# Optimization experiments

Measured on AMD Instinct MI355X. Metric: run time of the kernel, lower is better.

Reference implementation:

```python
import jax, jax.numpy as jnp
import numpy as np
import math

D_EMBED = 128   # per-head dim (config.d_embed)
N_HEADS = 12
ROPE_BASE = 10000.0


def rope(x):
    # x: [B, H, S, D]; interleaved-pair rotary embedding on last dim
    B, H, S, D = x.shape
    half = D // 2
    inv_freq = 1.0 / (ROPE_BASE ** (jnp.arange(0, half, dtype=jnp.float32) * 2.0 / D))
    ang = jnp.arange(S, dtype=jnp.float32)[:, None] * inv_freq[None, :]  # [S, D/2]
    cos, sin = jnp.cos(ang), jnp.sin(ang)
    xp = x.reshape(B, H, S, half, 2)
    x1, x2 = xp[..., 0], xp[..., 1]
    o1 = x1 * cos - x2 * sin
    o2 = x1 * sin + x2 * cos
    return jnp.stack([o1, o2], axis=-1).reshape(B, H, S, D)


def setup_inputs() -> dict:
    key = jax.random.key(0)
    ks = jax.random.split(key, 5)
    B, S, E = 2, 2048, D_EMBED // 2
    inner = N_HEADS * D_EMBED
    sc = 0.02
    return {
        "q": jax.random.normal(ks[0], (B, S, E), dtype=jnp.float32),
        "Wq": jax.random.normal(ks[1], (inner, E), dtype=jnp.float32) * sc,
        "Wk": jax.random.normal(ks[2], (inner, E), dtype=jnp.float32) * sc,
        "Wv": jax.random.normal(ks[3], (inner, E), dtype=jnp.float32) * sc,
        "Wo": jax.random.normal(ks[4], (E, inner), dtype=jnp.float32) * sc,
    }


def reference(q, Wq, Wk, Wv, Wo):
    B, S, E = q.shape
    H, D = N_HEADS, D_EMBED
    scale = 1.0 / math.sqrt(D)

    def proj(x, W):
        return (x @ W.T).reshape(B, S, H, D).transpose(0, 2, 1, 3)  # [B,H,S,D]

    qh = rope(proj(q, Wq))
    kh = rope(proj(q, Wk))
    vh = proj(q, Wv)

    scores = jnp.einsum("bhsd,bhtd->bhst", qh, kh) * scale  # [B,H,S,S]
    causal = jnp.tril(jnp.ones((S, S), dtype=bool))
    scores = jnp.where(causal, scores, -jnp.inf)
    probs = jax.nn.softmax(scores, axis=-1)  # dropout omitted (eval mode)
    out = jnp.einsum("bhst,bhtd->bhsd", probs, vh)
    out = out.transpose(0, 2, 1, 3).reshape(B, S, H * D)
    return out @ Wo.T  # [B,S,E]
```

## Files before the change

### kernel.cpp

```cpp
#include <hip/hip_runtime.h>
#include <stdint.h>


typedef short v8s __attribute__((ext_vector_type(8)));
typedef unsigned int v4u __attribute__((ext_vector_type(4)));
typedef float v4f __attribute__((ext_vector_type(4)));
typedef float v16f __attribute__((ext_vector_type(16)));

#define MFMA16(a, b, c) __builtin_amdgcn_mfma_f32_16x16x32_bf16(a, b, c, 0, 0, 0)
#define MFMA32(a, b, c) __builtin_amdgcn_mfma_f32_32x32x16_bf16(a, b, c, 0, 0, 0)

#if __has_builtin(__builtin_amdgcn_exp2f)
#define EXP2(x) __builtin_amdgcn_exp2f(x)
#else
#define EXP2(x) exp2f(x)
#endif

#define SCALE2 (0.08838834764831845f * 1.4426950408889634f)

__device__ __forceinline__ unsigned short f2bf(float f) {
  uint32_t u = __builtin_bit_cast(uint32_t, f);
  u += 0x7FFFu + ((u >> 16) & 1u);
  return (unsigned short)(u >> 16);
}

__device__ __forceinline__ uint32_t packbf(float lo, float hi) {
  return __builtin_amdgcn_perm(__builtin_bit_cast(uint32_t, hi) + 0x8000u,
                               __builtin_bit_cast(uint32_t, lo) + 0x8000u,
                               0x07060302u);
}

__device__ __forceinline__ v16f zero16() {
  v16f z;
#pragma unroll
  for (int i = 0; i < 16; ++i) z[i] = 0.f;
  return z;
}

__device__ __forceinline__ void gl_lds16(const unsigned short* g, unsigned short* l) {
  __builtin_amdgcn_global_load_lds(
      (const __attribute__((address_space(1))) uint32_t*)g,
      (__attribute__((address_space(3))) uint32_t*)l, 16, 0, 0);
}

__global__ __launch_bounds__(256) void rope_table(float* __restrict__ cos_t,
                                                  float* __restrict__ sin_t) {
  int idx = blockIdx.x * 256 + threadIdx.x;
  if (idx >= 2048 * 64) return;
  int s = idx >> 6, f = idx & 63;
  float inv = exp2f((float)f * -0.20762050593046014f);
  float ang = (float)s * inv;
  float si, co;
  sincosf(ang, &si, &co);
  cos_t[idx] = co;
  sin_t[idx] = si;
}

__global__ __launch_bounds__(256) void proj_rope(
    const float* __restrict__ x, const float* __restrict__ Wq,
    const float* __restrict__ Wk, const float* __restrict__ Wv,
    const float* __restrict__ cos_t, const float* __restrict__ sin_t,
    unsigned short* __restrict__ qh, unsigned short* __restrict__ kh,
    unsigned short* __restrict__ vt) {
  const int wave = threadIdx.x >> 6, lane = threadIdx.x & 63;
  const int l16 = lane & 15, quad = lane >> 4;
  const int by = blockIdx.y;
  const int o_base = by * 64 + wave * 16;
  const int mat = o_base / 1536;
  const int inner0 = o_base % 1536;
  const int d0w = inner0 & 127;
  const float* Wsrc = (mat == 0) ? Wq : ((mat == 1) ? Wk : Wv);
  const float qscale = (mat == 0) ? SCALE2 : 1.0f;

  __shared__ __align__(16) unsigned short Lt[64][72];

  v8s wb[2];
  {
    const float* wr = Wsrc + (size_t)(inner0 + l16) * 64 + quad * 8;
#pragma unroll
    for (int s = 0; s < 2; ++s) {
      float4 a = *(const float4*)(wr + s * 32);
      float4 b = *(const float4*)(wr + s * 32 + 4);
      v8s t;
      t[0] = (short)f2bf(a.x); t[1] = (short)f2bf(a.y);
      t[2] = (short)f2bf(a.z); t[3] = (short)f2bf(a.w);
      t[4] = (short)f2bf(b.x); t[5] = (short)f2bf(b.y);
      t[6] = (short)f2bf(b.z); t[7] = (short)f2bf(b.w);
      wb[s] = t;
    }
  }

  const int d = d0w + l16;
  const int half = d >> 1;

#pragma unroll
  for (int i = 0; i < 4; ++i) {
    const int tok0 = blockIdx.x * 64 + i * 16;
    const float* xr = x + (size_t)(tok0 + l16) * 64 + quad * 8;
    v8s xa[2];
#pragma unroll
    for (int s = 0; s < 2; ++s) {
      float4 a = *(const float4*)(xr + s * 32);
      float4 b = *(const float4*)(xr + s * 32 + 4);
      v8s t;
      t[0] = (short)f2bf(a.x); t[1] = (short)f2bf(a.y);
      t[2] = (short)f2bf(a.z); t[3] = (short)f2bf(a.w);
      t[4] = (short)f2bf(b.x); t[5] = (short)f2bf(b.y);
      t[6] = (short)f2bf(b.z); t[7] = (short)f2bf(b.w);
      xa[s] = t;
    }
    v4f acc = {0.f, 0.f, 0.f, 0.f};
    acc = MFMA16(xa[0], wb[0], acc);
    acc = MFMA16(xa[1], wb[1], acc);

    if (mat < 2) {
#pragma unroll
      for (int r = 0; r < 4; ++r) {
        int sidx = (tok0 + quad * 4 + r) & 2047;
        float val = acc[r];
        float prt = __shfl_xor(val, 1);
        float co = cos_t[sidx * 64 + half];
        float si = sin_t[sidx * 64 + half];
        float rot = ((d & 1) == 0) ? (val * co - prt * si)
                                   : (prt * si + val * co);
        Lt[i * 16 + quad * 4 + r][wave * 16 + l16] = f2bf(rot * qscale);
      }
    } else {
#pragma unroll
      for (int r = 0; r < 4; ++r)
        Lt[wave * 16 + l16][i * 16 + quad * 4 + r] = f2bf(acc[r]);
    }
  }
  __syncthreads();

  const int matb = (by * 64) / 1536;
  const int innerb = (by * 64) % 1536;
  const int hb = innerb >> 7;
  const int d0b = innerb & 127;
  const int b = (blockIdx.x * 64) >> 11;
  const int tokbase = (blockIdx.x * 64) & 2047;
#pragma unroll
  for (int jj = 0; jj < 2; ++jj) {
    int cid = jj * 256 + threadIdx.x;
    int outer = cid >> 3, ic = cid & 7;
    v8s val = *(const v8s*)&Lt[outer][ic * 8];
    if (matb < 2) {
      unsigned short* dst = (matb == 0 ? qh : kh) +
          (((size_t)(b * 12 + hb)) * 2048 + tokbase + outer) * 128 + d0b + ic * 8;
      *(v8s*)dst = val;
    } else {
      const int kt = tokbase >> 6;
      const int G = ic >> 1, hhb = ic & 1;
      const int dd = d0b + outer;
      unsigned short* dst = vt +
          ((((((size_t)(b * 12 + hb)) * 32 + kt) * 4 + G) * 4 + (dd >> 5)) * 64 +
           hhb * 32 + (dd & 31)) * 8;
      *(v8s*)dst = val;
    }
  }
}

__global__ __launch_bounds__(256, 2) void attn(
    const unsigned short* __restrict__ qh, const unsigned short* __restrict__ kh,
    const unsigned short* __restrict__ vtf, unsigned short* __restrict__ att,
    const float* __restrict__ Wo, unsigned short* __restrict__ wob) {
  const int bh = blockIdx.x;
  const int qb = 15 - (int)blockIdx.y;
  const int t = threadIdx.x;
  const int lane = t & 63;
  const int l31 = lane & 31, hh = lane >> 5;
  const int w = t >> 6;
  const int r0w = qb * 128 + w * 32;
  const int qrow = r0w + l31;
  const int rowmax = r0w + 31;

  const unsigned short* Qb = qh + (size_t)bh * 2048 * 128;
  const unsigned short* Kb = kh + (size_t)bh * 2048 * 128;
  const unsigned short* Vb = vtf + (size_t)bh * 262144;

  __shared__ __align__(16) unsigned short Ktile[3][64 * 128];

  v8s qa[8];
  {
    const unsigned short* qr = Qb + (size_t)(r0w + l31) * 128 + hh * 8;
#pragma unroll
    for (int ks = 0; ks < 8; ++ks) qa[ks] = *(const v8s*)(qr + ks * 16);
  }

  int offK[4], ldsO[4];
#pragma unroll
  for (int i = 0; i < 4; ++i) {
    int flat = i * 256 + t;
    int kr = flat >> 4, kc = flat & 15;
    offK[i] = kr * 128 + ((kc ^ (kr & 15)) << 3);
    ldsO[i] = flat << 3;
  }
  auto stageK = [&](int kt, int buf) {
    const unsigned short* kg = Kb + ((size_t)(kt << 6)) * 128;
#pragma unroll
    for (int i = 0; i < 4; ++i) gl_lds16(kg + offK[i], &Ktile[buf][ldsO[i]]);
  };

  v16f O[4];
#pragma unroll
  for (int i = 0; i < 4; ++i) O[i] = zero16();
  float lsum = 0.f;

  const int nkt = 2 * qb + 2;
  stageK(0, 0);
  stageK(1, 1);
  asm volatile("s_waitcnt vmcnt(4)" ::: "memory");

  for (int kt = 0; kt < nkt; ++kt) {
    __builtin_amdgcn_s_barrier();
    __builtin_amdgcn_sched_barrier(0);
    const int key0 = kt << 6;
    const bool active = key0 <= rowmax;
    const bool hi = (key0 + 32) <= rowmax;

    v8s v0a[4], v0b[4], v1a[4], v1b[4];
    if (active) {
      const unsigned short* Vt = Vb + (size_t)kt * 8192;
#pragma unroll
      for (int dt = 0; dt < 4; ++dt)
        v0a[dt] = *(const v8s*)(Vt + ((0 * 4 + dt) * 64 + lane) * 8);
#pragma unroll
      for (int dt = 0; dt < 4; ++dt)
        v0b[dt] = *(const v8s*)(Vt + ((1 * 4 + dt) * 64 + lane) * 8);
      if (hi) {
#pragma unroll
        for (int dt = 0; dt < 4; ++dt)
          v1a[dt] = *(const v8s*)(Vt + ((2 * 4 + dt) * 64 + lane) * 8);
#pragma unroll
        for (int dt = 0; dt < 4; ++dt)
          v1b[dt] = *(const v8s*)(Vt + ((3 * 4 + dt) * 64 + lane) * 8);
      }
    }
    __builtin_amdgcn_sched_barrier(0);

    if (kt + 2 < nkt) stageK(kt + 2, (kt + 2) % 3);
    __builtin_amdgcn_sched_barrier(0);

    if (!active) {
      if (kt + 2 < nkt) asm volatile("s_waitcnt vmcnt(4)" ::: "memory");
      else              asm volatile("s_waitcnt vmcnt(0)" ::: "memory");
      continue;
    }

    const unsigned short* Kl = Ktile[kt % 3];
    const bool mask0 = (key0 + 31) > r0w;
    const bool mask1 = (key0 + 63) > r0w;

    auto softpack = [&](const v16f& SS, const v16f& ST, int kh2, bool needmask,
                        uint32_t* W) {
#pragma unroll
      for (int m = 0; m < 8; ++m) {
        float pa = EXP2(SS[2 * m] + ST[2 * m]);
        float pb = EXP2(SS[2 * m + 1] + ST[2 * m + 1]);
        if (needmask) {
          int keyb = key0 + kh2 * 32 + 2 * (m & 1) + 8 * (m >> 1) + 4 * hh;
          pa = (keyb <= qrow) ? pa : 0.f;
          pb = (keyb + 1 <= qrow) ? pb : 0.f;
        }
        lsum += pa + pb;
        W[m] = packbf(pa, pb);
      }
    };
    auto pvhalf = [&](const uint32_t* W, int kh2, const v8s* vA, const v8s* vB) {
      uint32_t r0 = __shfl_xor(hh ? W[0] : W[2], 32);
      uint32_t r1 = __shfl_xor(hh ? W[1] : W[3], 32);
      uint32_t r2 = __shfl_xor(hh ? W[4] : W[6], 32);
      uint32_t r3 = __shfl_xor(hh ? W[5] : W[7], 32);
#pragma unroll
      for (int gl = 0; gl < 2; ++gl) {
        const int g = kh2 * 2 + gl;
        if (key0 + g * 16 > rowmax) continue;
        uint32_t rA = gl ? r2 : r0, rB = gl ? r3 : r1;
        v4u fw;
        fw.x = hh ? rA : W[4 * gl];
        fw.y = hh ? rB : W[4 * gl + 1];
        fw.z = hh ? W[4 * gl + 2] : rA;
        fw.w = hh ? W[4 * gl + 3] : rB;
        v8s pfrag = __builtin_bit_cast(v8s, fw);
        const v8s* vv = gl ? vB : vA;
        __builtin_amdgcn_s_setprio(1);
#pragma unroll
        for (int dt = 0; dt < 4; ++dt) O[dt] = MFMA32(vv[dt], pfrag, O[dt]);
        __builtin_amdgcn_s_setprio(0);
      }
    };

    v16f Sa = zero16(), Sb = zero16();
    __builtin_amdgcn_s_setprio(1);
#pragma unroll
    for (int ks = 0; ks < 8; ks += 2) {
      v8s ka0 = *(const v8s*)(
          Kl + ((l31 * 16 + ((2 * ks + hh) ^ (l31 & 15))) << 3));
      v8s ka1 = *(const v8s*)(
          Kl + ((l31 * 16 + ((2 * ks + 2 + hh) ^ (l31 & 15))) << 3));
      Sa = MFMA32(ka0, qa[ks], Sa);
      Sb = MFMA32(ka1, qa[ks + 1], Sb);
    }
    __builtin_amdgcn_s_setprio(0);
    uint32_t W0[8];
    softpack(Sa, Sb, 0, mask0, W0);
    pvhalf(W0, 0, v0a, v0b);

    if (hi) {
      v16f Sc = zero16(), Sd = zero16();
      __builtin_amdgcn_s_setprio(1);
#pragma unroll
      for (int ks = 0; ks < 8; ks += 2) {
        v8s ka0 = *(const v8s*)(
            Kl + (((32 + l31) * 16 + ((2 * ks + hh) ^ (l31 & 15))) << 3));
        v8s ka1 = *(const v8s*)(
            Kl + (((32 + l31) * 16 + ((2 * ks + 2 + hh) ^ (l31 & 15))) << 3));
        Sc = MFMA32(ka0, qa[ks], Sc);
        Sd = MFMA32(ka1, qa[ks + 1], Sd);
      }
      __builtin_amdgcn_s_setprio(0);
      uint32_t W1[8];
      softpack(Sc, Sd, 1, mask1, W1);
      pvhalf(W1, 1, v1a, v1b);
    }
  }

  float tot = lsum + __shfl_xor(lsum, 32);
  float inv = 1.0f / tot;
  const int b = bh / 12, hq = bh % 12;
  unsigned short* arow = att + ((size_t)b * 2048 + qrow) * 1536 + hq * 128;
#pragma unroll
  for (int dt = 0; dt < 4; ++dt) {
#pragma unroll
    for (int pr = 0; pr < 4; ++pr) {
      float a0 = O[dt][4 * pr + 0] * inv, a1 = O[dt][4 * pr + 1] * inv;
      float a2 = O[dt][4 * pr + 2] * inv, a3 = O[dt][4 * pr + 3] * inv;
      uint2 uu;
      uu.x = packbf(a0, a1);
      uu.y = packbf(a2, a3);
      *(uint2*)(arow + dt * 32 + 8 * pr + 4 * hh) = uu;
    }
  }

  if (qb == 0) {
    const int base = bh * 4096;
#pragma unroll
    for (int i = 0; i < 16; ++i) wob[base + i * 256 + t] = f2bf(Wo[base + i * 256 + t]);
  }
}

__global__ __launch_bounds__(256) void outproj(
    const unsigned short* __restrict__ att, const unsigned short* __restrict__ wob,
    float* __restrict__ out) {
  const int wave = threadIdx.x >> 6, lane = threadIdx.x & 63;
  const int l16 = lane & 15, quad = lane >> 4;
  const int tok0 = blockIdx.x * 16;
  const int e0 = wave * 16;

  v4f acc0 = {0.f, 0.f, 0.f, 0.f}, acc1 = {0.f, 0.f, 0.f, 0.f};
  const unsigned short* ar = att + (size_t)(tok0 + l16) * 1536 + quad * 8;
  const unsigned short* wr = wob + (size_t)(e0 + l16) * 1536 + quad * 8;
#pragma unroll 4
  for (int s = 0; s < 24; ++s) {
    v8s a0 = *(const v8s*)(ar + (2 * s) * 32);
    v8s b0 = *(const v8s*)(wr + (2 * s) * 32);
    v8s a1 = *(const v8s*)(ar + (2 * s + 1) * 32);
    v8s b1 = *(const v8s*)(wr + (2 * s + 1) * 32);
    acc0 = MFMA16(a0, b0, acc0);
    acc1 = MFMA16(a1, b1, acc1);
  }
#pragma unroll
  for (int r = 0; r < 4; ++r)
    out[(size_t)(tok0 + quad * 4 + r) * 64 + e0 + l16] = acc0[r] + acc1[r];
}

extern "C" void kernel_launch(void* const* d_in, const int* in_sizes, int n_in,
                              void* d_out, int out_size, void* d_ws,
                              size_t ws_size, hipStream_t stream) {
  const float* q  = (const float*)d_in[0];
  const float* Wq = (const float*)d_in[1];
  const float* Wk = (const float*)d_in[2];
  const float* Wv = (const float*)d_in[3];
  const float* Wo = (const float*)d_in[4];
  float* out = (float*)d_out;

  unsigned short* ws = (unsigned short*)d_ws;
  unsigned short* qh  = ws;
  unsigned short* kh  = ws + 6291456;
  unsigned short* vtf = ws + 12582912;
  unsigned short* att = ws + 18874368;
  float* cos_t = (float*)((char*)d_ws + 50331648);
  float* sin_t = cos_t + 131072;
  unsigned short* wob = (unsigned short*)cos_t;

  rope_table<<<512, 256, 0, stream>>>(cos_t, sin_t);
  proj_rope<<<dim3(64, 72), 256, 0, stream>>>(q, Wq, Wk, Wv, cos_t, sin_t,
                                              qh, kh, vtf);
  attn<<<dim3(24, 16), 256, 0, stream>>>(qh, kh, vtf, att, Wo, wob);
  outproj<<<256, 256, 0, stream>>>(att, wob, out);
}
```

Baseline: 200.9 us.

## Split attention KV range across two wave groups with LDS reduction

Doubles the attention block to 512 threads: two groups of four waves each process half of the causal key tiles for the same 128 query rows, with each group staging its own K tiles into LDS. The partial O accumulators and row sums from the second group are written to swizzled LDS and added by the first group before normalisation and the bf16 store. This halves the serial key-loop length per block to reduce latency on the long causal rows, at the cost of more LDS, a full vmcnt(0) wait every iteration (less prefetch overlap), and an extra reduction step.

After: 424.4 us. 111% more time.

```diff
diff --git a/kernel.cpp b/kernel.cpp
--- a/kernel.cpp
+++ b/kernel.cpp
@@ -160,7 +160,7 @@
   }
 }
 
-__global__ __launch_bounds__(256, 2) void attn(
+__global__ __launch_bounds__(512, 4) void attn(
     const unsigned short* __restrict__ qh, const unsigned short* __restrict__ kh,
     const unsigned short* __restrict__ vtf, unsigned short* __restrict__ att,
     const float* __restrict__ Wo, unsigned short* __restrict__ wob) {
@@ -170,7 +170,8 @@
   const int lane = t & 63;
   const int l31 = lane & 31, hh = lane >> 5;
   const int w = t >> 6;
-  const int r0w = qb * 128 + w * 32;
+  const int rg = w & 3, kherd = w >> 2;
+  const int r0w = qb * 128 + rg * 32;
   const int qrow = r0w + l31;
   const int rowmax = r0w + 31;
 
@@ -178,27 +179,28 @@
   const unsigned short* Kb = kh + (size_t)bh * 2048 * 128;
   const unsigned short* Vb = vtf + (size_t)bh * 262144;
 
-  __shared__ __align__(16) unsigned short Ktile[3][64 * 128];
+  __shared__ __align__(16) unsigned short KSH[4 * 8192 + 512];
 
   v8s qa[8];
   {
-    const unsigned short* qr = Qb + (size_t)(r0w + l31) * 128 + hh * 8;
+    const unsigned short* qr = Qb + (size_t)qrow * 128 + hh * 8;
 #pragma unroll
     for (int ks = 0; ks < 8; ++ks) qa[ks] = *(const v8s*)(qr + ks * 16);
   }
 
-  int offK[4], ldsO[4];
-#pragma unroll
-  for (int i = 0; i < 4; ++i) {
-    int flat = i * 256 + t;
+  int offK[2];
+#pragma unroll
+  for (int i2 = 0; i2 < 2; ++i2) {
+    int flat = i2 * 512 + t;
     int kr = flat >> 4, kc = flat & 15;
-    offK[i] = kr * 128 + ((kc ^ (kr & 15)) << 3);
-    ldsO[i] = flat << 3;
-  }
-  auto stageK = [&](int kt, int buf) {
-    const unsigned short* kg = Kb + ((size_t)(kt << 6)) * 128;
-#pragma unroll
-    for (int i = 0; i < 4; ++i) gl_lds16(kg + offK[i], &Ktile[buf][ldsO[i]]);
+    offK[i2] = kr * 128 + ((kc ^ (kr & 15)) << 3);
+  }
+  auto stageT = [&](int ktile, int slot) {
+    const unsigned short* kg = Kb + ((size_t)(ktile << 6)) * 128;
+    unsigned short* db = &KSH[slot * 8192];
+#pragma unroll
+    for (int i2 = 0; i2 < 2; ++i2)
+      gl_lds16(kg + offK[i2], db + ((i2 * 512 + t) << 3));
   };
 
   v16f O[4];
@@ -206,14 +208,15 @@
   for (int i = 0; i < 4; ++i) O[i] = zero16();
   float lsum = 0.f;
 
-  const int nkt = 2 * qb + 2;
-  stageK(0, 0);
-  stageK(1, 1);
-  asm volatile("s_waitcnt vmcnt(4)" ::: "memory");
-
-  for (int kt = 0; kt < nkt; ++kt) {
+  const int NS = qb + 1;
+  stageT(0, 0);
+  stageT(qb + 1, 2);
+  asm volatile("s_waitcnt vmcnt(0)" ::: "memory");
+
+  for (int i = 0; i < NS; ++i) {
     __builtin_amdgcn_s_barrier();
     __builtin_amdgcn_sched_barrier(0);
+    const int kt = kherd ? (qb + 1 + i) : i;
     const int key0 = kt << 6;
     const bool active = key0 <= rowmax;
     const bool hi = (key0 + 32) <= rowmax;
@@ -238,114 +241,140 @@
     }
     __builtin_amdgcn_sched_barrier(0);
 
-    if (kt + 2 < nkt) stageK(kt + 2, (kt + 2) % 3);
+    if (i + 1 < NS) {
+      stageT(i + 1, (i + 1) & 1);
+      stageT(qb + 2 + i, 2 + ((i + 1) & 1));
+    }
     __builtin_amdgcn_sched_barrier(0);
 
-    if (!active) {
-      if (kt + 2 < nkt) asm volatile("s_waitcnt vmcnt(4)" ::: "memory");
-      else              asm volatile("s_waitcnt vmcnt(0)" ::: "memory");
-      continue;
-    }
-
-    const unsigned short* Kl = Ktile[kt % 3];
-    const bool mask0 = (key0 + 31) > r0w;
-    const bool mask1 = (key0 + 63) > r0w;
-
-    auto softpack = [&](const v16f& SS, const v16f& ST, int kh2, bool needmask,
-                        uint32_t* W) {
-#pragma unroll
-      for (int m = 0; m < 8; ++m) {
-        float pa = EXP2(SS[2 * m] + ST[2 * m]);
-        float pb = EXP2(SS[2 * m + 1] + ST[2 * m + 1]);
-        if (needmask) {
-          int keyb = key0 + kh2 * 32 + 2 * (m & 1) + 8 * (m >> 1) + 4 * hh;
-          pa = (keyb <= qrow) ? pa : 0.f;
-          pb = (keyb + 1 <= qrow) ? pb : 0.f;
+    if (active) {
+      const unsigned short* Kl = &KSH[(kherd * 2 + (i & 1)) * 8192];
+      const bool mask0 = (key0 + 31) > r0w;
+      const bool mask1 = (key0 + 63) > r0w;
+
+      auto softpack = [&](const v16f& SS, const v16f& ST, int kh2, bool needmask,
+                          uint32_t* W) {
+#pragma unroll
+        for (int m = 0; m < 8; ++m) {
+          float pa = EXP2(SS[2 * m] + ST[2 * m]);
+          float pb = EXP2(SS[2 * m + 1] + ST[2 * m + 1]);
+          if (needmask) {
+            int keyb = key0 + kh2 * 32 + 2 * (m & 1) + 8 * (m >> 1) + 4 * hh;
+            pa = (keyb <= qrow) ? pa : 0.f;
+            pb = (keyb + 1 <= qrow) ? pb : 0.f;
+          }
+          lsum += pa + pb;
+          W[m] = packbf(pa, pb);
         }
-        lsum += pa + pb;
-        W[m] = packbf(pa, pb);
-      }
-    };
-    auto pvhalf = [&](const uint32_t* W, int kh2, const v8s* vA, const v8s* vB) {
-      uint32_t r0 = __shfl_xor(hh ? W[0] : W[2], 32);
-      uint32_t r1 = __shfl_xor(hh ? W[1] : W[3], 32);
-      uint32_t r2 = __shfl_xor(hh ? W[4] : W[6], 32);
-      uint32_t r3 = __shfl_xor(hh ? W[5] : W[7], 32);
-#pragma unroll
-      for (int gl = 0; gl < 2; ++gl) {
-        const int g = kh2 * 2 + gl;
-        if (key0 + g * 16 > rowmax) continue;
-        uint32_t rA = gl ? r2 : r0, rB = gl ? r3 : r1;
-        v4u fw;
-        fw.x = hh ? rA : W[4 * gl];
-        fw.y = hh ? rB : W[4 * gl + 1];
-        fw.z = hh ? W[4 * gl + 2] : rA;
-        fw.w = hh ? W[4 * gl + 3] : rB;
-        v8s pfrag = __builtin_bit_cast(v8s, fw);
-        const v8s* vv = gl ? vB : vA;
-        __builtin_amdgcn_s_setprio(1);
-#pragma unroll
-        for (int dt = 0; dt < 4; ++dt) O[dt] = MFMA32(vv[dt], pfrag, O[dt]);
-        __builtin_amdgcn_s_setprio(0);
-      }
-    };
-
-    v16f Sa = zero16(), Sb = zero16();
-    __builtin_amdgcn_s_setprio(1);
-#pragma unroll
-    for (int ks = 0; ks < 8; ks += 2) {
-      v8s ka0 = *(const v8s*)(
-          Kl + ((l31 * 16 + ((2 * ks + hh) ^ (l31 & 15))) << 3));
-      v8s ka1 = *(const v8s*)(
-          Kl + ((l31 * 16 + ((2 * ks + 2 + hh) ^ (l31 & 15))) << 3));
-      Sa = MFMA32(ka0, qa[ks], Sa);
-      Sb = MFMA32(ka1, qa[ks + 1], Sb);
-    }
-    __builtin_amdgcn_s_setprio(0);
-    uint32_t W0[8];
-    softpack(Sa, Sb, 0, mask0, W0);
-    pvhalf(W0, 0, v0a, v0b);
-
-    if (hi) {
-      v16f Sc = zero16(), Sd = zero16();
+      };
+      auto pvhalf = [&](const uint32_t* W, int kh2, const v8s* vA, const v8s* vB) {
+        uint32_t r0 = __shfl_xor(hh ? W[0] : W[2], 32);
+        uint32_t r1 = __shfl_xor(hh ? W[1] : W[3], 32);
+        uint32_t r2 = __shfl_xor(hh ? W[4] : W[6], 32);
+        uint32_t r3 = __shfl_xor(hh ? W[5] : W[7], 32);
+#pragma unroll
+        for (int gl = 0; gl < 2; ++gl) {
+          const int g = kh2 * 2 + gl;
+          if (key0 + g * 16 > rowmax) continue;
+          uint32_t rA = gl ? r2 : r0, rB = gl ? r3 : r1;
+          v4u fw;
+          fw.x = hh ? rA : W[4 * gl];
+          fw.y = hh ? rB : W[4 * gl + 1];
+          fw.z = hh ? W[4 * gl + 2] : rA;
+          fw.w = hh ? W[4 * gl + 3] : rB;
+          v8s pfrag = __builtin_bit_cast(v8s, fw);
+          const v8s* vv = gl ? vB : vA;
+          __builtin_amdgcn_s_setprio(1);
+#pragma unroll
+          for (int dt = 0; dt < 4; ++dt) O[dt] = MFMA32(vv[dt], pfrag, O[dt]);
+          __builtin_amdgcn_s_setprio(0);
+        }
+      };
+
+      v16f Sa = zero16(), Sb = zero16();
       __builtin_amdgcn_s_setprio(1);
 #pragma unroll
       for (int ks = 0; ks < 8; ks += 2) {
         v8s ka0 = *(const v8s*)(
-            Kl + (((32 + l31) * 16 + ((2 * ks + hh) ^ (l31 & 15))) << 3));
+            Kl + ((l31 * 16 + ((2 * ks + hh) ^ (l31 & 15))) << 3));
         v8s ka1 = *(const v8s*)(
-            Kl + (((32 + l31) * 16 + ((2 * ks + 2 + hh) ^ (l31 & 15))) << 3));
-        Sc = MFMA32(ka0, qa[ks], Sc);
-        Sd = MFMA32(ka1, qa[ks + 1], Sd);
+            Kl + ((l31 * 16 + ((2 * ks + 2 + hh) ^ (l31 & 15))) << 3));
+        Sa = MFMA32(ka0, qa[ks], Sa);
+        Sb = MFMA32(ka1, qa[ks + 1], Sb);
       }
       __builtin_amdgcn_s_setprio(0);
-      uint32_t W1[8];
-      softpack(Sc, Sd, 1, mask1, W1);
-      pvhalf(W1, 1, v1a, v1b);
-    }
-  }
-
-  float tot = lsum + __shfl_xor(lsum, 32);
-  float inv = 1.0f / tot;
-  const int b = bh / 12, hq = bh % 12;
-  unsigned short* arow = att + ((size_t)b * 2048 + qrow) * 1536 + hq * 128;
-#pragma unroll
-  for (int dt = 0; dt < 4; ++dt) {
-#pragma unroll
-    for (int pr = 0; pr < 4; ++pr) {
-      float a0 = O[dt][4 * pr + 0] * inv, a1 = O[dt][4 * pr + 1] * inv;
-      float a2 = O[dt][4 * pr + 2] * inv, a3 = O[dt][4 * pr + 3] * inv;
-      uint2 uu;
-      uu.x = packbf(a0, a1);
-      uu.y = packbf(a2, a3);
-      *(uint2*)(arow + dt * 32 + 8 * pr + 4 * hh) = uu;
+      uint32_t W0[8];
+      softpack(Sa, Sb, 0, mask0, W0);
+      pvhalf(W0, 0, v0a, v0b);
+
+      if (hi) {
+        v16f Sc = zero16(), Sd = zero16();
+        __builtin_amdgcn_s_setprio(1);
+#pragma unroll
+        for (int ks = 0; ks < 8; ks += 2) {
+          v8s ka0 = *(const v8s*)(
+              Kl + (((32 + l31) * 16 + ((2 * ks + hh) ^ (l31 & 15))) << 3));
+          v8s ka1 = *(const v8s*)(
+              Kl + (((32 + l31) * 16 + ((2 * ks + 2 + hh) ^ (l31 & 15))) << 3));
+          Sc = MFMA32(ka0, qa[ks], Sc);
+          Sd = MFMA32(ka1, qa[ks + 1], Sd);
+        }
+        __builtin_amdgcn_s_setprio(0);
+        uint32_t W1[8];
+        softpack(Sc, Sd, 1, mask1, W1);
+        pvhalf(W1, 1, v1a, v1b);
+      }
+    }
+    asm volatile("s_waitcnt vmcnt(0)" ::: "memory");
+  }
+
+  __syncthreads();
+  float* Ored = (float*)KSH;
+  float* lred = (float*)(KSH + 32768);
+  if (kherd == 1) {
+    float* baseO = Ored + rg * 4096 + l31 * 128;
+#pragma unroll
+    for (int dt = 0; dt < 4; ++dt)
+#pragma unroll
+      for (int pr = 0; pr < 4; ++pr) {
+        float4 v;
+        v.x = O[dt][4 * pr + 0]; v.y = O[dt][4 * pr + 1];
+        v.z = O[dt][4 * pr + 2]; v.w = O[dt][4 * pr + 3];
+        *(float4*)(baseO + dt * 32 + (((2 * pr + hh) ^ (l31 & 7)) << 2)) = v;
+      }
+    lred[rg * 64 + lane] = lsum;
+  }
+  __syncthreads();
+  if (kherd == 0) {
+    const float lt = lsum + lred[rg * 64 + lane];
+    const float tot = lt + __shfl_xor(lt, 32);
+    const float inv = 1.0f / tot;
+    const int b = bh / 12, hq = bh % 12;
+    unsigned short* arow = att + ((size_t)b * 2048 + qrow) * 1536 + hq * 128;
+    const float* baseO = Ored + rg * 4096 + l31 * 128;
+#pragma unroll
+    for (int dt = 0; dt < 4; ++dt) {
+#pragma unroll
+      for (int pr = 0; pr < 4; ++pr) {
+        float4 v = *(const float4*)(
+            baseO + dt * 32 + (((2 * pr + hh) ^ (l31 & 7)) << 2));
+        float a0 = (O[dt][4 * pr + 0] + v.x) * inv;
+        float a1 = (O[dt][4 * pr + 1] + v.y) * inv;
+        float a2 = (O[dt][4 * pr + 2] + v.z) * inv;
+        float a3 = (O[dt][4 * pr + 3] + v.w) * inv;
+        uint2 uu;
+        uu.x = packbf(a0, a1);
+        uu.y = packbf(a2, a3);
+        *(uint2*)(arow + dt * 32 + 8 * pr + 4 * hh) = uu;
+      }
     }
   }
 
   if (qb == 0) {
     const int base = bh * 4096;
 #pragma unroll
-    for (int i = 0; i < 16; ++i) wob[base + i * 256 + t] = f2bf(Wo[base + i * 256 + t]);
+    for (int i = 0; i < 8; ++i)
+      wob[base + i * 512 + t] = f2bf(Wo[base + i * 512 + t]);
   }
 }
 
@@ -396,6 +425,6 @@
   rope_table<<<512, 256, 0, stream>>>(cos_t, sin_t);
   proj_rope<<<dim3(64, 72), 256, 0, stream>>>(q, Wq, Wk, Wv, cos_t, sin_t,
                                               qh, kh, vtf);
-  attn<<<dim3(24, 16), 256, 0, stream>>>(qh, kh, vtf, att, Wo, wob);
+  attn<<<dim3(24, 16), 512, 0, stream>>>(qh, kh, vtf, att, Wo, wob);
   outproj<<<256, 256, 0, stream>>>(att, wob, out);
 }
```
